# Kernel tuning notes

Measured on AMD Instinct MI355X. Metric: run time of the kernel, lower is better.

Reference implementation:

```python
import jax, jax.numpy as jnp
import numpy as np

VOCAB = 5000; EMB = 300; AUDIO = 74; HID = 128
D1 = 16; D2 = 16; DIM = D1 * D2
UNITS = 128; CELL = 64; OUT = 1
B = 32; S = 32
NGRAMS = (1, 3)


def _lstm(x, w_ih, w_hh, b_ih, b_hh):
    # PyTorch LSTMCell semantics, gate order i, f, g, o
    Bb = x.shape[0]; H = w_hh.shape[1]
    def step(carry, xt):
        h, c = carry
        gates = xt @ w_ih.T + h @ w_hh.T + b_ih + b_hh
        i, f, g, o = jnp.split(gates, 4, axis=-1)
        c = jax.nn.sigmoid(f) * c + jax.nn.sigmoid(i) * jnp.tanh(g)
        h = jax.nn.sigmoid(o) * jnp.tanh(c)
        return (h, c), h
    init = (jnp.zeros((Bb, H), x.dtype), jnp.zeros((Bb, H), x.dtype))
    _, hs = jax.lax.scan(step, init, jnp.swapaxes(x, 0, 1))
    return jnp.swapaxes(hs, 0, 1)  # (B, S, H)


def _windows(x, n):
    # zero-padded n-gram windows: (B, S, d) -> (B, S, n, d)
    xp = jnp.pad(x, ((0, 0), (0, n - 1), (0, 0)))
    s = x.shape[1]
    return jnp.stack([xp[:, k:k + s, :] for k in range(n)], axis=2)


def setup_inputs() -> dict:
    key = jax.random.key(0)
    ks = jax.random.split(key, 26)
    g = lambda i, shape, sc=0.05: jax.random.normal(ks[i], shape, dtype=jnp.float32) * sc
    return dict(
        word_indexes=jax.random.randint(ks[0], (B, S), 0, VOCAB),
        audio=jax.random.normal(ks[1], (B, S, AUDIO), dtype=jnp.float32),
        lookup_table=g(2, (VOCAB, EMB), 0.5),
        phase_tab0=g(3, (VOCAB, D1), 3.14),
        phase_tab1=g(4, (VOCAB, D2), 3.14),
        w_ih=g(5, (4 * HID, EMB)), w_hh=g(6, (4 * HID, HID)),
        b_ih=g(7, (4 * HID,)), b_hh=g(8, (4 * HID,)),
        w_lin=g(9, (D1, HID)), b_lin=g(10, (D1,)),
        w1=g(11, (D2, AUDIO)), b1=g(12, (D2,)),
        w2=g(13, (D2, D2)), b2=g(14, (D2,)),
        w3=g(15, (D2, D2)), b3=g(16, (D2,)),
        modality_weights=jnp.zeros((2,), jnp.float32),
        meas_r=g(17, (UNITS, DIM), 0.5), meas_i=g(18, (UNITS, DIM), 0.5),
        fw1=g(19, (CELL, UNITS)), fb1=g(20, (CELL,)),
        fw2=g(21, (CELL, CELL)), fb2=g(22, (CELL,)),
        fw3=g(23, (OUT, CELL)), fb3=jnp.zeros((OUT,), jnp.float32),
    )


def reference(word_indexes, audio, lookup_table, phase_tab0, phase_tab1,
              w_ih, w_hh, b_ih, b_hh, w_lin, b_lin,
              w1, b1, w2, b2, w3, b3,
              modality_weights, meas_r, meas_i,
              fw1, fb1, fw2, fb2, fw3, fb3):
    eps = 1e-10
    # amplitude subnets (dropout rates are 0 / eval mode)
    text = lookup_table[word_indexes]                      # (B,S,EMB)
    h = _lstm(text, w_ih, w_hh, b_ih, b_hh)
    amp0 = h @ w_lin.T + b_lin                             # (B,S,D1)
    a = jax.nn.relu(audio @ w1.T + b1)
    a = jax.nn.relu(a @ w2.T + b2)
    amp1 = jax.nn.relu(a @ w3.T + b3)                      # (B,S,D2)
    ph0 = phase_tab0[word_indexes]
    ph1 = phase_tab1[word_indexes]

    def branch(amp, ph):
        norm = jnp.linalg.norm(amp, axis=-1, keepdims=True)
        ampn = amp / (norm + eps)
        return norm, ampn * jnp.cos(ph), ampn * jnp.sin(ph)

    n0, r0, i0 = branch(amp0, ph0)
    n1, r1, i1 = branch(amp1, ph1)
    mw = jax.nn.softmax(modality_weights)
    weight = mw[0] * n0 + mw[1] * n1                       # (B,S,1)

    # sequential complex tensor product across modalities,
    # starting from (real=1, imag=1) as in the original code
    tpr = r0 - i0
    tpi = r0 + i0
    real = jnp.einsum('bsi,bsj->bsij', tpr, r1) - jnp.einsum('bsi,bsj->bsij', tpi, i1)
    imag = jnp.einsum('bsi,bsj->bsij', tpr, i1) + jnp.einsum('bsi,bsj->bsij', tpi, r1)
    real = real.reshape(B, S, DIM)
    imag = imag.reshape(B, S, DIM)

    # measurement kernel: unit-norm complex vectors
    kn = jnp.sqrt(jnp.sum(meas_r ** 2 + meas_i ** 2, axis=-1, keepdims=True)) + eps
    vr = meas_r / kn
    vi = meas_i / kn

    probs = []
    for n in NGRAMS:
        wr = _windows(real, n)                             # (B,S,n,DIM)
        wi = _windows(imag, n)
        ww = jax.nn.softmax(_windows(weight, n)[..., 0], axis=-1)  # (B,S,n)
        # complex mixture: rho = sum_n w_n |v_n><v_n|
        rho_r = (jnp.einsum('bsn,bsni,bsnj->bsij', ww, wr, wr)
                 + jnp.einsum('bsn,bsni,bsnj->bsij', ww, wi, wi))
        rho_i = (jnp.einsum('bsn,bsni,bsnj->bsij', ww, wi, wr)
                 - jnp.einsum('bsn,bsni,bsnj->bsij', ww, wr, wi))
        # measurement: Re(v^H rho v) per unit
        m = (jnp.einsum('bsij,ui,uj->bsu', rho_r, vr, vr)
             + jnp.einsum('bsij,ui,uj->bsu', rho_r, vi, vi)
             + jnp.einsum('bsij,ui,uj->bsu', rho_i, vi, vr)
             - jnp.einsum('bsij,ui,uj->bsu', rho_i, vr, vi))
        probs.append(m)
    probs = jnp.concatenate(probs, axis=1)                 # (B, S*len(NGRAMS), UNITS)
    feat = jnp.max(probs, axis=1)                          # 'max' pooling
    y = jax.nn.relu(feat @ fw1.T + fb1)
    y = jax.nn.relu(y @ fw2.T + fb2)
    return y @ fw3.T + fb3                                 # (B, OUT)
```

## Files before the change

### kernel.cpp

```cpp
#include <hip/hip_runtime.h>
#include <math.h>


static constexpr unsigned XW0_OFF  = 0u;
static constexpr unsigned XW1_OFF  = 524288u;
static constexpr unsigned HOUT_OFF = 1048576u;
static constexpr unsigned XMAT_OFF = HOUT_OFF + 131072u;
static constexpr unsigned WT_OFF   = XMAT_OFF + 524288u;
static constexpr unsigned VPP_OFF  = WT_OFF + 1024u;
static constexpr unsigned PP_OFF   = VPP_OFF + 131072u;
static constexpr unsigned PP_HALF  = 262144u;

__global__ __launch_bounds__(256) void k1_xw_gemm(
    const int* __restrict__ widx, const float* __restrict__ lut,
    const float* __restrict__ w_ih, const float* __restrict__ b_ih,
    const float* __restrict__ b_hh,
    const float* __restrict__ mr, const float* __restrict__ mi,
    float* __restrict__ ws)
{
  const int bid = blockIdx.x;
  const int t = threadIdx.x;

  if (bid >= 256) {
    const int u = bid - 256;
    float r  = mr[u * 256 + t];
    float ii = mi[u * 256 + t];
    float sq = r * r + ii * ii;
    #pragma unroll
    for (int off = 1; off < 64; off <<= 1) sq += __shfl_xor(sq, off);
    __shared__ float wsum[4];
    if ((t & 63) == 0) wsum[t >> 6] = sq;
    __syncthreads();
    float tot = wsum[0] + wsum[1] + wsum[2] + wsum[3];
    float inv = 1.0f / (sqrtf(tot) + 1e-10f);
    float vr = r * inv, vi = ii * inv;
    float* vpp = ws + VPP_OFF;
    vpp[(2 * u) * 512 + t]           = vr;
    vpp[(2 * u) * 512 + 256 + t]     = vi;
    vpp[(2 * u + 1) * 512 + t]       = -vi;
    vpp[(2 * u + 1) * 512 + 256 + t] = vr;
    return;
  }

  const int rb = bid & 15, cb = (bid >> 4) & 7, kq = bid >> 7;
  const int R = rb * 64, C = cb * 64;
  const int kbase_g = kq * 152;
  const int ktot = kq ? 148 : 152;

  __shared__ alignas(16) float As[32][68];
  __shared__ alignas(16) float Ws[32][68];

  float acc[4][4] = {};
  const int r0 = (t & 15) * 4, j0 = (t >> 4) * 4;

  for (int kt = 0; kt < 5; ++kt) {
    int kl = ktot - kt * 32; if (kl > 32) kl = 32;
    #pragma unroll
    for (int pass = 0; pass < 2; ++pass) {
      int rr = (t >> 3) + pass * 32;
      int kk4 = (t & 7) * 4;
      float4 av = make_float4(0.f, 0.f, 0.f, 0.f);
      float4 wv = make_float4(0.f, 0.f, 0.f, 0.f);
      if (kk4 < kl) {
        int gk = kbase_g + kt * 32 + kk4;
        int word = widx[R + rr];
        av = *(const float4*)&lut[word * 300 + gk];
        wv = *(const float4*)&w_ih[(C + rr) * 300 + gk];
      }
      As[kk4 + 0][rr] = av.x; As[kk4 + 1][rr] = av.y;
      As[kk4 + 2][rr] = av.z; As[kk4 + 3][rr] = av.w;
      Ws[kk4 + 0][rr] = wv.x; Ws[kk4 + 1][rr] = wv.y;
      Ws[kk4 + 2][rr] = wv.z; Ws[kk4 + 3][rr] = wv.w;
    }
    __syncthreads();
    #pragma unroll
    for (int k = 0; k < 32; ++k) {
      float4 a4 = *(const float4*)&As[k][r0];
      float4 w4 = *(const float4*)&Ws[k][j0];
      float ar[4] = {a4.x, a4.y, a4.z, a4.w};
      float wr[4] = {w4.x, w4.y, w4.z, w4.w};
      #pragma unroll
      for (int i2 = 0; i2 < 4; ++i2)
        #pragma unroll
        for (int j2 = 0; j2 < 4; ++j2)
          acc[i2][j2] = fmaf(ar[i2], wr[j2], acc[i2][j2]);
    }
    __syncthreads();
  }

  float* xw = ws + (kq ? XW1_OFF : XW0_OFF);
  #pragma unroll
  for (int i2 = 0; i2 < 4; ++i2) {
    int row = R + r0 + i2, col = C + j0;
    float4 v = make_float4(acc[i2][0], acc[i2][1], acc[i2][2], acc[i2][3]);
    if (kq == 0) {
      v.x += b_ih[col + 0] + b_hh[col + 0];
      v.y += b_ih[col + 1] + b_hh[col + 1];
      v.z += b_ih[col + 2] + b_hh[col + 2];
      v.w += b_ih[col + 3] + b_hh[col + 3];
    }
    *(float4*)&xw[row * 512 + col] = v;
  }
}

__global__ __launch_bounds__(640, 1) void k2_lstm_mix(
    const float* __restrict__ w_hh, const int* __restrict__ widx,
    const float* __restrict__ audio,
    const float* __restrict__ ph0t, const float* __restrict__ ph1t,
    const float* __restrict__ w_lin, const float* __restrict__ b_lin,
    const float* __restrict__ w1, const float* __restrict__ b1,
    const float* __restrict__ w2, const float* __restrict__ b2,
    const float* __restrict__ w3, const float* __restrict__ b3,
    const float* __restrict__ modw, float* __restrict__ ws)
{
  const int b = blockIdx.x;
  const int t = threadIdx.x;
  const int wv = t >> 6;
  const int l  = t & 63;

  __shared__ alignas(16) float part[8][512];
  __shared__ alignas(16) float hist[33][128];
  __shared__ float amp0s[32][17], a1s[32][17], a2s[32][17], amp1s[32][17];
  __shared__ float tprs[32][17], tpis[32][17], r1ss[32][17], i1ss[32][17];
  __shared__ float nrm0[32], nrm1[32];

  const float* xw0 = ws + XW0_OFF;
  const float* xw1 = ws + XW1_OFF;

  if (t < 128) hist[0][t] = 0.f;

  if (wv < 8) {
    float4 wA[4][4], wB[4][4];
    #pragma unroll
    for (int g = 0; g < 4; ++g) {
      const float* pA = w_hh + (g * 128 + l) * 128 + wv * 16;
      const float* pB = w_hh + (g * 128 + 64 + l) * 128 + wv * 16;
      #pragma unroll
      for (int c = 0; c < 4; ++c) {
        wA[g][c] = *(const float4*)&pA[c * 4];
        wB[g][c] = *(const float4*)&pB[c * 4];
      }
    }
    #pragma unroll
    for (int g = 0; g < 4; ++g)
      #pragma unroll
      for (int c = 0; c < 4; ++c) {
        asm volatile("" : "+v"(wA[g][c].x), "+v"(wA[g][c].y), "+v"(wA[g][c].z), "+v"(wA[g][c].w));
        asm volatile("" : "+v"(wB[g][c].x), "+v"(wB[g][c].y), "+v"(wB[g][c].z), "+v"(wB[g][c].w));
      }
    __syncthreads();
    for (int s = 0; s < 32; ++s) {
      const float* hb = &hist[s][wv * 16];
      float aA0 = 0.f, aA1 = 0.f, aA2 = 0.f, aA3 = 0.f;
      float aB0 = 0.f, aB1 = 0.f, aB2 = 0.f, aB3 = 0.f;
      #pragma unroll
      for (int c = 0; c < 4; ++c) {
        float4 h4 = *(const float4*)&hb[c * 4];
        aA0 = fmaf(wA[0][c].x, h4.x, fmaf(wA[0][c].y, h4.y, fmaf(wA[0][c].z, h4.z, fmaf(wA[0][c].w, h4.w, aA0))));
        aA1 = fmaf(wA[1][c].x, h4.x, fmaf(wA[1][c].y, h4.y, fmaf(wA[1][c].z, h4.z, fmaf(wA[1][c].w, h4.w, aA1))));
        aA2 = fmaf(wA[2][c].x, h4.x, fmaf(wA[2][c].y, h4.y, fmaf(wA[2][c].z, h4.z, fmaf(wA[2][c].w, h4.w, aA2))));
        aA3 = fmaf(wA[3][c].x, h4.x, fmaf(wA[3][c].y, h4.y, fmaf(wA[3][c].z, h4.z, fmaf(wA[3][c].w, h4.w, aA3))));
        aB0 = fmaf(wB[0][c].x, h4.x, fmaf(wB[0][c].y, h4.y, fmaf(wB[0][c].z, h4.z, fmaf(wB[0][c].w, h4.w, aB0))));
        aB1 = fmaf(wB[1][c].x, h4.x, fmaf(wB[1][c].y, h4.y, fmaf(wB[1][c].z, h4.z, fmaf(wB[1][c].w, h4.w, aB1))));
        aB2 = fmaf(wB[2][c].x, h4.x, fmaf(wB[2][c].y, h4.y, fmaf(wB[2][c].z, h4.z, fmaf(wB[2][c].w, h4.w, aB2))));
        aB3 = fmaf(wB[3][c].x, h4.x, fmaf(wB[3][c].y, h4.y, fmaf(wB[3][c].z, h4.z, fmaf(wB[3][c].w, h4.w, aB3))));
      }
      *(float4*)&part[wv][l * 4]       = make_float4(aA0, aA1, aA2, aA3);
      *(float4*)&part[wv][256 + l * 4] = make_float4(aB0, aB1, aB2, aB3);
      __syncthreads();
      __syncthreads();
    }
  } else {
    const int jj = (wv - 8) * 64 + l;
    float c = 0.f;
    __syncthreads();
    for (int s = 0; s < 32; ++s) {
      const int base = (b * 32 + s) * 512 + jj;
      float x0 = xw0[base +   0] + xw1[base +   0];
      float x1 = xw0[base + 128] + xw1[base + 128];
      float x2 = xw0[base + 256] + xw1[base + 256];
      float x3 = xw0[base + 384] + xw1[base + 384];
      __syncthreads();
      float g0 = x0, g1 = x1, g2 = x2, g3 = x3;
      #pragma unroll
      for (int w = 0; w < 8; ++w) {
        float4 p = *(const float4*)&part[w][jj * 4];
        g0 += p.x; g1 += p.y; g2 += p.z; g3 += p.w;
      }
      float si = 1.f / (1.f + __expf(-g0));
      float sf = 1.f / (1.f + __expf(-g1));
      float tg = 1.f - 2.f / (1.f + __expf(2.f * g2));
      float so = 1.f / (1.f + __expf(-g3));
      c = sf * c + si * tg;
      float tc = 1.f - 2.f / (1.f + __expf(2.f * c));
      hist[s + 1][jj] = so * tc;
      __syncthreads();
    }
  }

  const int word_base = b * 32;
  if (t < 512) {
    const int s = t >> 4, d = t & 15;
    float acc = b_lin[d];
    const float* wl = w_lin + d * 128;
    const float* hh = hist[s + 1];
    for (int u = 0; u < 128; ++u) acc = fmaf(hh[u], wl[u], acc);
    amp0s[s][d] = acc;
    float a = b1[d];
    const float* au = audio + (word_base + s) * 74;
    const float* w1r = w1 + d * 74;
    for (int k = 0; k < 74; ++k) a = fmaf(au[k], w1r[k], a);
    a1s[s][d] = fmaxf(a, 0.f);
  }
  __syncthreads();
  if (t < 512) {
    const int s = t >> 4, d = t & 15;
    float a = b2[d];
    #pragma unroll
    for (int k = 0; k < 16; ++k) a = fmaf(a1s[s][k], w2[d * 16 + k], a);
    a2s[s][d] = fmaxf(a, 0.f);
  }
  __syncthreads();
  if (t < 512) {
    const int s = t >> 4, d = t & 15;
    float a = b3[d];
    #pragma unroll
    for (int k = 0; k < 16; ++k) a = fmaf(a2s[s][k], w3[d * 16 + k], a);
    amp1s[s][d] = fmaxf(a, 0.f);
  }
  __syncthreads();
  if (t < 32) {
    float sq = 0.f;
    #pragma unroll
    for (int d = 0; d < 16; ++d) sq += amp0s[t][d] * amp0s[t][d];
    nrm0[t] = sqrtf(sq);
  } else if (t >= 64 && t < 96) {
    int s = t - 64;
    float sq = 0.f;
    #pragma unroll
    for (int d = 0; d < 16; ++d) sq += amp1s[s][d] * amp1s[s][d];
    nrm1[s] = sqrtf(sq);
  }
  __syncthreads();
  if (t < 512) {
    const int s = t >> 4, d = t & 15;
    const int word = widx[word_base + s];
    float k0 = amp0s[s][d] / (nrm0[s] + 1e-10f);
    float ph = ph0t[word * 16 + d];
    float cc = cosf(ph), sn = sinf(ph);
    tprs[s][d] = k0 * (cc - sn);
    tpis[s][d] = k0 * (cc + sn);
    float k1v = amp1s[s][d] / (nrm1[s] + 1e-10f);
    float p1 = ph1t[word * 16 + d];
    r1ss[s][d] = k1v * cosf(p1);
    i1ss[s][d] = k1v * sinf(p1);
  } else if (t >= 512 && t < 544) {
    int s = t - 512;
    float e0 = __expf(modw[0]), e1 = __expf(modw[1]);
    float mw0 = e0 / (e0 + e1);
    ws[WT_OFF + word_base + s] = mw0 * nrm0[s] + (1.f - mw0) * nrm1[s];
  }
  __syncthreads();
  if (t < 512) {
    float* X = ws + XMAT_OFF;
    const int c2 = t;
    const int half = c2 >> 8;
    const int i2 = (c2 >> 4) & 15, j2 = c2 & 15;
    for (int s = 0; s < 32; ++s) {
      float v;
      if (half == 0) v = tprs[s][i2] * r1ss[s][j2] - tpis[s][i2] * i1ss[s][j2];
      else           v = tprs[s][i2] * i1ss[s][j2] + tpis[s][i2] * r1ss[s][j2];
      X[(word_base + s) * 512 + c2] = v;
    }
  }
}

__global__ __launch_bounds__(256) void k4_meas(float* __restrict__ ws)
{
  const int bid = blockIdx.x, t = threadIdx.x;
  const int rb = bid & 15, cb = (bid >> 4) & 3, kq = bid >> 6;
  const int R = rb * 64, C = cb * 64;
  const float* X = ws + XMAT_OFF;
  const float* V = ws + VPP_OFF;
  __shared__ alignas(16) float Xs[32][68];
  __shared__ alignas(16) float Vs[32][68];
  float acc[4][4] = {};
  const int r0 = (t & 15) * 4, j0 = (t >> 4) * 4;

  for (int kt = 0; kt < 4; ++kt) {
    #pragma unroll
    for (int pass = 0; pass < 2; ++pass) {
      int rr = (t >> 3) + pass * 32;
      int kk4 = (t & 7) * 4;
      int gk = kq * 128 + kt * 32 + kk4;
      float4 xv = *(const float4*)&X[(R + rr) * 512 + gk];
      float4 vv = *(const float4*)&V[(C + rr) * 512 + gk];
      Xs[kk4 + 0][rr] = xv.x; Xs[kk4 + 1][rr] = xv.y;
      Xs[kk4 + 2][rr] = xv.z; Xs[kk4 + 3][rr] = xv.w;
      Vs[kk4 + 0][rr] = vv.x; Vs[kk4 + 1][rr] = vv.y;
      Vs[kk4 + 2][rr] = vv.z; Vs[kk4 + 3][rr] = vv.w;
    }
    __syncthreads();
    #pragma unroll
    for (int k = 0; k < 32; ++k) {
      float4 a4 = *(const float4*)&Xs[k][r0];
      float4 w4 = *(const float4*)&Vs[k][j0];
      float ar[4] = {a4.x, a4.y, a4.z, a4.w};
      float wr[4] = {w4.x, w4.y, w4.z, w4.w};
      #pragma unroll
      for (int i2 = 0; i2 < 4; ++i2)
        #pragma unroll
        for (int j2 = 0; j2 < 4; ++j2)
          acc[i2][j2] = fmaf(ar[i2], wr[j2], acc[i2][j2]);
    }
    __syncthreads();
  }
  float* Pp = ws + PP_OFF + (unsigned)kq * PP_HALF;
  #pragma unroll
  for (int i2 = 0; i2 < 4; ++i2) {
    float4 v = make_float4(acc[i2][0], acc[i2][1], acc[i2][2], acc[i2][3]);
    *(float4*)&Pp[(R + r0 + i2) * 256 + C + j0] = v;
  }
}

__global__ __launch_bounds__(512) void k5_final(
    const float* __restrict__ fw1, const float* __restrict__ fb1,
    const float* __restrict__ fw2, const float* __restrict__ fb2,
    const float* __restrict__ fw3, const float* __restrict__ fb3,
    const float* __restrict__ ws, float* __restrict__ out)
{
  const int b = blockIdx.x, t = threadIdx.x;
  const int u = t & 127, sg = t >> 7;
  __shared__ float ewt[34];
  __shared__ float pl[32][128];
  __shared__ float fred[4][128];
  __shared__ float feat[128], y1[64], y2[64];
  if (t < 32) ewt[t] = __expf(ws[WT_OFF + b * 32 + t]);
  if (t >= 32 && t < 34) ewt[t] = 1.f;
  __syncthreads();

  const float* Pp = ws + PP_OFF;
  #pragma unroll
  for (int i = 0; i < 8; ++i) {
    int s = sg * 8 + i;
    int bs = b * 32 + s;
    float A = 0.f, Bv = 0.f;
    #pragma unroll
    for (int kq = 0; kq < 4; ++kq) {
      A  += Pp[kq * PP_HALF + bs * 256 + 2 * u];
      Bv += Pp[kq * PP_HALF + bs * 256 + 2 * u + 1];
    }
    pl[s][u] = A * A + Bv * Bv;
  }
  __syncthreads();

  float m = -1e30f;
  #pragma unroll
  for (int i = 0; i < 8; ++i) {
    int s = sg * 8 + i;
    float p0 = pl[s][u];
    m = fmaxf(m, p0);
    float e0 = ewt[s], e1 = ewt[s + 1], e2 = ewt[s + 2];
    float num = e0 * p0;
    if (s + 1 < 32) num += e1 * pl[s + 1][u];
    if (s + 2 < 32) num += e2 * pl[s + 2][u];
    m = fmaxf(m, num / (e0 + e1 + e2));
  }
  fred[sg][u] = m;
  __syncthreads();
  if (t < 128)
    feat[t] = fmaxf(fmaxf(fred[0][t], fred[1][t]), fmaxf(fred[2][t], fred[3][t]));
  __syncthreads();
  if (t < 64) {
    float acc = fb1[t];
    for (int k = 0; k < 128; ++k) acc = fmaf(feat[k], fw1[t * 128 + k], acc);
    y1[t] = fmaxf(acc, 0.f);
  }
  __syncthreads();
  if (t < 64) {
    float acc = fb2[t];
    #pragma unroll
    for (int k = 0; k < 64; ++k) acc = fmaf(y1[k], fw2[t * 64 + k], acc);
    y2[t] = fmaxf(acc, 0.f);
  }
  __syncthreads();
  if (t == 0) {
    float acc = fb3[0];
    #pragma unroll
    for (int k = 0; k < 64; ++k) acc = fmaf(y2[k], fw3[k], acc);
    out[b] = acc;
  }
}

extern "C" void kernel_launch(void* const* d_in, const int* in_sizes, int n_in,
                              void* d_out, int out_size, void* d_ws, size_t ws_size,
                              hipStream_t stream) {
  const int*   widx  = (const int*)d_in[0];
  const float* audio = (const float*)d_in[1];
  const float* lut   = (const float*)d_in[2];
  const float* ph0   = (const float*)d_in[3];
  const float* ph1   = (const float*)d_in[4];
  const float* w_ih  = (const float*)d_in[5];
  const float* w_hh  = (const float*)d_in[6];
  const float* b_ih  = (const float*)d_in[7];
  const float* b_hh  = (const float*)d_in[8];
  const float* w_lin = (const float*)d_in[9];
  const float* b_lin = (const float*)d_in[10];
  const float* w1    = (const float*)d_in[11];
  const float* b1    = (const float*)d_in[12];
  const float* w2    = (const float*)d_in[13];
  const float* b2    = (const float*)d_in[14];
  const float* w3    = (const float*)d_in[15];
  const float* b3    = (const float*)d_in[16];
  const float* modw  = (const float*)d_in[17];
  const float* mr    = (const float*)d_in[18];
  const float* mi    = (const float*)d_in[19];
  const float* fw1   = (const float*)d_in[20];
  const float* fb1   = (const float*)d_in[21];
  const float* fw2   = (const float*)d_in[22];
  const float* fb2   = (const float*)d_in[23];
  const float* fw3   = (const float*)d_in[24];
  const float* fb3   = (const float*)d_in[25];
  float* ws  = (float*)d_ws;
  float* out = (float*)d_out;

  k1_xw_gemm<<<dim3(384), dim3(256), 0, stream>>>(widx, lut, w_ih, b_ih, b_hh, mr, mi, ws);
  k2_lstm_mix<<<dim3(32), dim3(640), 0, stream>>>(w_hh, widx, audio, ph0, ph1,
                                                  w_lin, b_lin, w1, b1, w2, b2,
                                                  w3, b3, modw, ws);
  k4_meas<<<dim3(256), dim3(256), 0, stream>>>(ws);
  k5_final<<<dim3(32), dim3(512), 0, stream>>>(fw1, fb1, fw2, fb2, fw3, fb3, ws, out);
}
```

Before: 190.7 us.

## Merge LSTM gate waves into matvec waves with double-buffered partials and staged weights

New measurement: 192.7 us. About the same (+1.0%).

```diff
diff --git a/kernel.cpp b/kernel.cpp
--- a/kernel.cpp
+++ b/kernel.cpp
@@ -4,12 +4,21 @@
 
 static constexpr unsigned XW0_OFF  = 0u;
 static constexpr unsigned XW1_OFF  = 524288u;
-static constexpr unsigned HOUT_OFF = 1048576u;
-static constexpr unsigned XMAT_OFF = HOUT_OFF + 131072u;
+static constexpr unsigned XMAT_OFF = 1179648u;
 static constexpr unsigned WT_OFF   = XMAT_OFF + 524288u;
 static constexpr unsigned VPP_OFF  = WT_OFF + 1024u;
 static constexpr unsigned PP_OFF   = VPP_OFF + 131072u;
 static constexpr unsigned PP_HALF  = 262144u;
+
+static constexpr int WLIN = 0;
+static constexpr int W1O  = 2048;
+static constexpr int W2O  = 3232;
+static constexpr int W3O  = 3488;
+static constexpr int AUDO = 3744;
+static constexpr int BLIN = 6112;
+static constexpr int B1O  = 6128;
+static constexpr int B2O  = 6144;
+static constexpr int B3O  = 6160;
 
 __global__ __launch_bounds__(256) void k1_xw_gemm(
     const int* __restrict__ widx, const float* __restrict__ lut,
@@ -103,7 +112,7 @@
   }
 }
 
-__global__ __launch_bounds__(640, 1) void k2_lstm_mix(
+__global__ __launch_bounds__(512, 2) void k2_lstm_mix(
     const float* __restrict__ w_hh, const int* __restrict__ widx,
     const float* __restrict__ audio,
     const float* __restrict__ ph0t, const float* __restrict__ ph1t,
@@ -118,8 +127,9 @@
   const int wv = t >> 6;
   const int l  = t & 63;
 
-  __shared__ alignas(16) float part[8][512];
-  __shared__ alignas(16) float hist[33][128];
+  __shared__ alignas(16) float part[2][8][512];
+  __shared__ alignas(16) float hist[33][132];
+  __shared__ float stage[6176];
   __shared__ float amp0s[32][17], a1s[32][17], a2s[32][17], amp1s[32][17];
   __shared__ float tprs[32][17], tpis[32][17], r1ss[32][17], i1ss[32][17];
   __shared__ float nrm0[32], nrm1[32];
@@ -127,64 +137,57 @@
   const float* xw0 = ws + XW0_OFF;
   const float* xw1 = ws + XW1_OFF;
 
+  float4 wA[4][4], wB[4][4];
+  #pragma unroll
+  for (int g = 0; g < 4; ++g) {
+    const float* pA = w_hh + (g * 128 + l) * 128 + wv * 16;
+    const float* pB = w_hh + (g * 128 + 64 + l) * 128 + wv * 16;
+    #pragma unroll
+    for (int c = 0; c < 4; ++c) {
+      wA[g][c] = *(const float4*)&pA[c * 4];
+      wB[g][c] = *(const float4*)&pB[c * 4];
+    }
+  }
+
+  const int ju = wv * 16 + (l & 15);
+  float c = 0.f;
+  float x0 = 0.f, x1 = 0.f, x2 = 0.f, x3 = 0.f;
+  if (l < 16) {
+    const int base = (b * 32 + 0) * 512 + ju;
+    x0 = xw0[base +   0] + xw1[base +   0];
+    x1 = xw0[base + 128] + xw1[base + 128];
+    x2 = xw0[base + 256] + xw1[base + 256];
+    x3 = xw0[base + 384] + xw1[base + 384];
+  }
   if (t < 128) hist[0][t] = 0.f;
-
-  if (wv < 8) {
-    float4 wA[4][4], wB[4][4];
-    #pragma unroll
-    for (int g = 0; g < 4; ++g) {
-      const float* pA = w_hh + (g * 128 + l) * 128 + wv * 16;
-      const float* pB = w_hh + (g * 128 + 64 + l) * 128 + wv * 16;
-      #pragma unroll
-      for (int c = 0; c < 4; ++c) {
-        wA[g][c] = *(const float4*)&pA[c * 4];
-        wB[g][c] = *(const float4*)&pB[c * 4];
-      }
-    }
-    #pragma unroll
-    for (int g = 0; g < 4; ++g)
-      #pragma unroll
-      for (int c = 0; c < 4; ++c) {
-        asm volatile("" : "+v"(wA[g][c].x), "+v"(wA[g][c].y), "+v"(wA[g][c].z), "+v"(wA[g][c].w));
-        asm volatile("" : "+v"(wB[g][c].x), "+v"(wB[g][c].y), "+v"(wB[g][c].z), "+v"(wB[g][c].w));
-      }
-    __syncthreads();
-    for (int s = 0; s < 32; ++s) {
-      const float* hb = &hist[s][wv * 16];
-      float aA0 = 0.f, aA1 = 0.f, aA2 = 0.f, aA3 = 0.f;
-      float aB0 = 0.f, aB1 = 0.f, aB2 = 0.f, aB3 = 0.f;
-      #pragma unroll
-      for (int c = 0; c < 4; ++c) {
-        float4 h4 = *(const float4*)&hb[c * 4];
-        aA0 = fmaf(wA[0][c].x, h4.x, fmaf(wA[0][c].y, h4.y, fmaf(wA[0][c].z, h4.z, fmaf(wA[0][c].w, h4.w, aA0))));
-        aA1 = fmaf(wA[1][c].x, h4.x, fmaf(wA[1][c].y, h4.y, fmaf(wA[1][c].z, h4.z, fmaf(wA[1][c].w, h4.w, aA1))));
-        aA2 = fmaf(wA[2][c].x, h4.x, fmaf(wA[2][c].y, h4.y, fmaf(wA[2][c].z, h4.z, fmaf(wA[2][c].w, h4.w, aA2))));
-        aA3 = fmaf(wA[3][c].x, h4.x, fmaf(wA[3][c].y, h4.y, fmaf(wA[3][c].z, h4.z, fmaf(wA[3][c].w, h4.w, aA3))));
-        aB0 = fmaf(wB[0][c].x, h4.x, fmaf(wB[0][c].y, h4.y, fmaf(wB[0][c].z, h4.z, fmaf(wB[0][c].w, h4.w, aB0))));
-        aB1 = fmaf(wB[1][c].x, h4.x, fmaf(wB[1][c].y, h4.y, fmaf(wB[1][c].z, h4.z, fmaf(wB[1][c].w, h4.w, aB1))));
-        aB2 = fmaf(wB[2][c].x, h4.x, fmaf(wB[2][c].y, h4.y, fmaf(wB[2][c].z, h4.z, fmaf(wB[2][c].w, h4.w, aB2))));
-        aB3 = fmaf(wB[3][c].x, h4.x, fmaf(wB[3][c].y, h4.y, fmaf(wB[3][c].z, h4.z, fmaf(wB[3][c].w, h4.w, aB3))));
-      }
-      *(float4*)&part[wv][l * 4]       = make_float4(aA0, aA1, aA2, aA3);
-      *(float4*)&part[wv][256 + l * 4] = make_float4(aB0, aB1, aB2, aB3);
-      __syncthreads();
-      __syncthreads();
-    }
-  } else {
-    const int jj = (wv - 8) * 64 + l;
-    float c = 0.f;
-    __syncthreads();
-    for (int s = 0; s < 32; ++s) {
-      const int base = (b * 32 + s) * 512 + jj;
-      float x0 = xw0[base +   0] + xw1[base +   0];
-      float x1 = xw0[base + 128] + xw1[base + 128];
-      float x2 = xw0[base + 256] + xw1[base + 256];
-      float x3 = xw0[base + 384] + xw1[base + 384];
-      __syncthreads();
+  __syncthreads();
+
+  {
+    const float* hb = &hist[0][wv * 16];
+    float aA0=0.f,aA1=0.f,aA2=0.f,aA3=0.f,aB0=0.f,aB1=0.f,aB2=0.f,aB3=0.f;
+    #pragma unroll
+    for (int cc = 0; cc < 4; ++cc) {
+      float4 h4 = *(const float4*)&hb[cc * 4];
+      aA0 = fmaf(wA[0][cc].x, h4.x, fmaf(wA[0][cc].y, h4.y, fmaf(wA[0][cc].z, h4.z, fmaf(wA[0][cc].w, h4.w, aA0))));
+      aA1 = fmaf(wA[1][cc].x, h4.x, fmaf(wA[1][cc].y, h4.y, fmaf(wA[1][cc].z, h4.z, fmaf(wA[1][cc].w, h4.w, aA1))));
+      aA2 = fmaf(wA[2][cc].x, h4.x, fmaf(wA[2][cc].y, h4.y, fmaf(wA[2][cc].z, h4.z, fmaf(wA[2][cc].w, h4.w, aA2))));
+      aA3 = fmaf(wA[3][cc].x, h4.x, fmaf(wA[3][cc].y, h4.y, fmaf(wA[3][cc].z, h4.z, fmaf(wA[3][cc].w, h4.w, aA3))));
+      aB0 = fmaf(wB[0][cc].x, h4.x, fmaf(wB[0][cc].y, h4.y, fmaf(wB[0][cc].z, h4.z, fmaf(wB[0][cc].w, h4.w, aB0))));
+      aB1 = fmaf(wB[1][cc].x, h4.x, fmaf(wB[1][cc].y, h4.y, fmaf(wB[1][cc].z, h4.z, fmaf(wB[1][cc].w, h4.w, aB1))));
+      aB2 = fmaf(wB[2][cc].x, h4.x, fmaf(wB[2][cc].y, h4.y, fmaf(wB[2][cc].z, h4.z, fmaf(wB[2][cc].w, h4.w, aB2))));
+      aB3 = fmaf(wB[3][cc].x, h4.x, fmaf(wB[3][cc].y, h4.y, fmaf(wB[3][cc].z, h4.z, fmaf(wB[3][cc].w, h4.w, aB3))));
+    }
+    *(float4*)&part[0][wv][l * 4]       = make_float4(aA0, aA1, aA2, aA3);
+    *(float4*)&part[0][wv][256 + l * 4] = make_float4(aB0, aB1, aB2, aB3);
+  }
+  __syncthreads();
+
+  for (int s = 0; s < 32; ++s) {
+    if (l < 16) {
       float g0 = x0, g1 = x1, g2 = x2, g3 = x3;
       #pragma unroll
       for (int w = 0; w < 8; ++w) {
-        float4 p = *(const float4*)&part[w][jj * 4];
+        float4 p = *(const float4*)&part[s & 1][w][ju * 4];
         g0 += p.x; g1 += p.y; g2 += p.z; g3 += p.w;
       }
       float si = 1.f / (1.f + __expf(-g0));
@@ -193,57 +196,95 @@
       float so = 1.f / (1.f + __expf(-g3));
       c = sf * c + si * tg;
       float tc = 1.f - 2.f / (1.f + __expf(2.f * c));
-      hist[s + 1][jj] = so * tc;
-      __syncthreads();
-    }
+      hist[s + 1][ju] = so * tc;
+      if (s < 31) {
+        const int nb = (b * 32 + s + 1) * 512 + ju;
+        x0 = xw0[nb +   0] + xw1[nb +   0];
+        x1 = xw0[nb + 128] + xw1[nb + 128];
+        x2 = xw0[nb + 256] + xw1[nb + 256];
+        x3 = xw0[nb + 384] + xw1[nb + 384];
+      }
+    }
+    if (s < 31) {
+      const float* hb = &hist[s + 1][wv * 16];
+      float aA0=0.f,aA1=0.f,aA2=0.f,aA3=0.f,aB0=0.f,aB1=0.f,aB2=0.f,aB3=0.f;
+      #pragma unroll
+      for (int cc = 0; cc < 4; ++cc) {
+        float4 h4 = *(const float4*)&hb[cc * 4];
+        aA0 = fmaf(wA[0][cc].x, h4.x, fmaf(wA[0][cc].y, h4.y, fmaf(wA[0][cc].z, h4.z, fmaf(wA[0][cc].w, h4.w, aA0))));
+        aA1 = fmaf(wA[1][cc].x, h4.x, fmaf(wA[1][cc].y, h4.y, fmaf(wA[1][cc].z, h4.z, fmaf(wA[1][cc].w, h4.w, aA1))));
+        aA2 = fmaf(wA[2][cc].x, h4.x, fmaf(wA[2][cc].y, h4.y, fmaf(wA[2][cc].z, h4.z, fmaf(wA[2][cc].w, h4.w, aA2))));
+        aA3 = fmaf(wA[3][cc].x, h4.x, fmaf(wA[3][cc].y, h4.y, fmaf(wA[3][cc].z, h4.z, fmaf(wA[3][cc].w, h4.w, aA3))));
+        aB0 = fmaf(wB[0][cc].x, h4.x, fmaf(wB[0][cc].y, h4.y, fmaf(wB[0][cc].z, h4.z, fmaf(wB[0][cc].w, h4.w, aB0))));
+        aB1 = fmaf(wB[1][cc].x, h4.x, fmaf(wB[1][cc].y, h4.y, fmaf(wB[1][cc].z, h4.z, fmaf(wB[1][cc].w, h4.w, aB1))));
+        aB2 = fmaf(wB[2][cc].x, h4.x, fmaf(wB[2][cc].y, h4.y, fmaf(wB[2][cc].z, h4.z, fmaf(wB[2][cc].w, h4.w, aB2))));
+        aB3 = fmaf(wB[3][cc].x, h4.x, fmaf(wB[3][cc].y, h4.y, fmaf(wB[3][cc].z, h4.z, fmaf(wB[3][cc].w, h4.w, aB3))));
+      }
+      *(float4*)&part[(s + 1) & 1][wv][l * 4]       = make_float4(aA0, aA1, aA2, aA3);
+      *(float4*)&part[(s + 1) & 1][wv][256 + l * 4] = make_float4(aB0, aB1, aB2, aB3);
+    }
+    __syncthreads();
   }
 
   const int word_base = b * 32;
-  if (t < 512) {
-    const int s = t >> 4, d = t & 15;
-    float acc = b_lin[d];
-    const float* wl = w_lin + d * 128;
-    const float* hh = hist[s + 1];
+  for (int i = t; i < 1544; i += 512) {
+    const float* src;
+    if (i < 512)       src = w_lin + i * 4;
+    else if (i < 808)  src = w1 + (i - 512) * 4;
+    else if (i < 872)  src = w2 + (i - 808) * 4;
+    else if (i < 936)  src = w3 + (i - 872) * 4;
+    else if (i < 1528) src = audio + word_base * 74 + (i - 936) * 4;
+    else {
+      int j = i - 1528;
+      const float* bsrc = (j < 4) ? b_lin : (j < 8) ? b1 : (j < 12) ? b2 : b3;
+      src = bsrc + (j & 3) * 4;
+    }
+    *(float4*)&stage[i * 4] = *(const float4*)src;
+  }
+  __syncthreads();
+
+  const int s = t >> 4, d = t & 15;
+  {
+    float acc = stage[BLIN + d];
+    const float* wl = &stage[WLIN + d * 128];
+    const float* hh = &hist[s + 1][0];
     for (int u = 0; u < 128; ++u) acc = fmaf(hh[u], wl[u], acc);
     amp0s[s][d] = acc;
-    float a = b1[d];
-    const float* au = audio + (word_base + s) * 74;
-    const float* w1r = w1 + d * 74;
+    float a = stage[B1O + d];
+    const float* au = &stage[AUDO + s * 74];
+    const float* w1r = &stage[W1O + d * 74];
     for (int k = 0; k < 74; ++k) a = fmaf(au[k], w1r[k], a);
     a1s[s][d] = fmaxf(a, 0.f);
   }
   __syncthreads();
-  if (t < 512) {
-    const int s = t >> 4, d = t & 15;
-    float a = b2[d];
-    #pragma unroll
-    for (int k = 0; k < 16; ++k) a = fmaf(a1s[s][k], w2[d * 16 + k], a);
+  {
+    float a = stage[B2O + d];
+    #pragma unroll
+    for (int k = 0; k < 16; ++k) a = fmaf(a1s[s][k], stage[W2O + d * 16 + k], a);
     a2s[s][d] = fmaxf(a, 0.f);
   }
   __syncthreads();
-  if (t < 512) {
-    const int s = t >> 4, d = t & 15;
-    float a = b3[d];
-    #pragma unroll
-    for (int k = 0; k < 16; ++k) a = fmaf(a2s[s][k], w3[d * 16 + k], a);
+  {
+    float a = stage[B3O + d];
+    #pragma unroll
+    for (int k = 0; k < 16; ++k) a = fmaf(a2s[s][k], stage[W3O + d * 16 + k], a);
     amp1s[s][d] = fmaxf(a, 0.f);
   }
   __syncthreads();
   if (t < 32) {
     float sq = 0.f;
     #pragma unroll
-    for (int d = 0; d < 16; ++d) sq += amp0s[t][d] * amp0s[t][d];
+    for (int dd = 0; dd < 16; ++dd) sq += amp0s[t][dd] * amp0s[t][dd];
     nrm0[t] = sqrtf(sq);
   } else if (t >= 64 && t < 96) {
-    int s = t - 64;
+    int ss = t - 64;
     float sq = 0.f;
     #pragma unroll
-    for (int d = 0; d < 16; ++d) sq += amp1s[s][d] * amp1s[s][d];
-    nrm1[s] = sqrtf(sq);
-  }
-  __syncthreads();
-  if (t < 512) {
-    const int s = t >> 4, d = t & 15;
+    for (int dd = 0; dd < 16; ++dd) sq += amp1s[ss][dd] * amp1s[ss][dd];
+    nrm1[ss] = sqrtf(sq);
+  }
+  __syncthreads();
+  {
     const int word = widx[word_base + s];
     float k0 = amp0s[s][d] / (nrm0[s] + 1e-10f);
     float ph = ph0t[word * 16 + d];
@@ -254,23 +295,23 @@
     float p1 = ph1t[word * 16 + d];
     r1ss[s][d] = k1v * cosf(p1);
     i1ss[s][d] = k1v * sinf(p1);
-  } else if (t >= 512 && t < 544) {
-    int s = t - 512;
-    float e0 = __expf(modw[0]), e1 = __expf(modw[1]);
-    float mw0 = e0 / (e0 + e1);
-    ws[WT_OFF + word_base + s] = mw0 * nrm0[s] + (1.f - mw0) * nrm1[s];
-  }
-  __syncthreads();
-  if (t < 512) {
+    if (d == 0) {
+      float e0 = __expf(modw[0]), e1 = __expf(modw[1]);
+      float mw0 = e0 / (e0 + e1);
+      ws[WT_OFF + word_base + s] = mw0 * nrm0[s] + (1.f - mw0) * nrm1[s];
+    }
+  }
+  __syncthreads();
+  {
     float* X = ws + XMAT_OFF;
     const int c2 = t;
     const int half = c2 >> 8;
     const int i2 = (c2 >> 4) & 15, j2 = c2 & 15;
-    for (int s = 0; s < 32; ++s) {
+    for (int ss = 0; ss < 32; ++ss) {
       float v;
-      if (half == 0) v = tprs[s][i2] * r1ss[s][j2] - tpis[s][i2] * i1ss[s][j2];
-      else           v = tprs[s][i2] * i1ss[s][j2] + tpis[s][i2] * r1ss[s][j2];
-      X[(word_base + s) * 512 + c2] = v;
+      if (half == 0) v = tprs[ss][i2] * r1ss[ss][j2] - tpis[ss][i2] * i1ss[ss][j2];
+      else           v = tprs[ss][i2] * i1ss[ss][j2] + tpis[ss][i2] * r1ss[ss][j2];
+      X[(word_base + ss) * 512 + c2] = v;
     }
   }
 }
@@ -425,7 +466,7 @@
   float* out = (float*)d_out;
 
   k1_xw_gemm<<<dim3(384), dim3(256), 0, stream>>>(widx, lut, w_ih, b_ih, b_hh, mr, mi, ws);
-  k2_lstm_mix<<<dim3(32), dim3(640), 0, stream>>>(w_hh, widx, audio, ph0, ph1,
+  k2_lstm_mix<<<dim3(32), dim3(512), 0, stream>>>(w_hh, widx, audio, ph0, ph1,
                                                   w_lin, b_lin, w1, b1, w2, b2,
                                                   w3, b3, modw, ws);
   k4_meas<<<dim3(256), dim3(256), 0, stream>>>(ws);
```
